# Kernel optimization log

Hardware: AMD Instinct MI355X
Metric: run time of the kernel (lower is better)

Reference implementation:

```python
import jax, jax.numpy as jnp
import numpy as np
from jax import lax

T_STEPS = 16
TAU = 2.0
ALPHA = 4.0  # sigmoid surrogate sharpness
BN_EPS = 1e-5


def conv1d(x, w, b, stride, pad):
    # x: [N,C,L], w: [O,I,K]
    y = lax.conv_general_dilated(x, w, (stride,), [(pad, pad)],
                                 dimension_numbers=('NCH', 'OIH', 'NCH'))
    return y + b[None, :, None]


def maxpool1d(x):  # kernel 3, stride 2, pad 1 (pad value -inf via init)
    return lax.reduce_window(x, -jnp.inf, lax.max, (1, 1, 3), (1, 1, 2),
                             [(0, 0), (0, 0), (1, 1)])


def spike(x):  # heaviside forward (surrogate only matters for bwd)
    return (x >= 0).astype(x.dtype)


def lif(x_seq):
    # multi-step LIF: v += (x - v)/tau (v_reset=0), spike at v>=1, hard reset, detach_reset
    def step(v, x):
        v = v + (x - v) / TAU
        s = spike(v - 1.0)
        v = v * (1.0 - lax.stop_gradient(s))
        return v, s
    _, s_seq = lax.scan(step, jnp.zeros_like(x_seq[0]), x_seq)
    return s_seq


def seq_apply(f, xs):
    # apply stateless layer over [T,B,...] by folding T into batch
    T, B = xs.shape[0], xs.shape[1]
    y = f(xs.reshape((T * B,) + xs.shape[2:]))
    return y.reshape((T, B) + y.shape[1:])


def setup_inputs() -> dict:
    key = jax.random.key(0)
    ks = jax.random.split(key, 12)
    B, L = 256, 4097
    inp = {
        'x': jax.random.normal(ks[0], (B, L), jnp.float32),
        'conv0_w': jax.random.normal(ks[1], (16, 1, 7), jnp.float32) * 0.2,
        'conv0_b': jax.random.normal(ks[2], (16,), jnp.float32) * 0.1,
        'bn_g': jnp.ones((16,), jnp.float32),
        'bn_b': jnp.zeros((16,), jnp.float32),
        'bn_m': jax.random.normal(ks[3], (16,), jnp.float32) * 0.1,
        'bn_v': jnp.ones((16,), jnp.float32),
        'conv1_w': jax.random.normal(ks[4], (32, 16, 5), jnp.float32) * 0.1,
        'conv1_b': jax.random.normal(ks[5], (32,), jnp.float32) * 0.1,
        'conv2_w': jax.random.normal(ks[6], (64, 32, 3), jnp.float32) * 0.1,
        'conv2_b': jax.random.normal(ks[7], (64,), jnp.float32) * 0.1,
        'fc1_w': jax.random.normal(ks[8], (32, 64), jnp.float32) * 0.12,
        'fc1_b': jax.random.normal(ks[9], (32,), jnp.float32) * 0.1,
        'fc2_w': jax.random.normal(ks[10], (5, 32), jnp.float32) * 0.17,
        'fc2_b': jax.random.normal(ks[11], (5,), jnp.float32) * 0.1,
    }
    return inp


def reference(x, conv0_w, conv0_b, bn_g, bn_b, bn_m, bn_v,
              conv1_w, conv1_b, conv2_w, conv2_b,
              fc1_w, fc1_b, fc2_w, fc2_b):
    # ---- static encoder ----
    h = x[:, None, :]                                  # [B,1,4097]
    h = conv1d(h, conv0_w, conv0_b, 2, 3)              # [B,16,2049]
    h = (h - bn_m[None, :, None]) * lax.rsqrt(bn_v + BN_EPS)[None, :, None] \
        * bn_g[None, :, None] + bn_b[None, :, None]
    h = jax.nn.relu(h)
    h = maxpool1d(h)                                   # [B,16,1025]
    # ---- repeat over T timesteps ----
    hs = jnp.broadcast_to(h[None], (T_STEPS,) + h.shape)  # [T,B,16,1025]
    # ---- spiking trunk ----
    hs = seq_apply(lambda a: conv1d(a, conv1_w, conv1_b, 2, 2), hs)  # [T,B,32,513]
    hs = lif(hs)
    hs = seq_apply(maxpool1d, hs)                      # [T,B,32,257]
    hs = seq_apply(lambda a: conv1d(a, conv2_w, conv2_b, 2, 1), hs)  # [T,B,64,129]
    hs = lif(hs)
    # dropout: identity (inference); adaptive avg pool to 1 + flatten
    hs = hs.mean(axis=-1)                              # [T,B,64]
    # ---- classifier ----
    hs = jnp.einsum('tbd,od->tbo', hs, fc1_w) + fc1_b  # [T,B,32]
    hs = lif(hs)
    hs = jnp.einsum('tbd,od->tbo', hs, fc2_w) + fc2_b  # [T,B,5]
    return hs.mean(axis=0)                             # [B,5]
```

## Files before the change

kernel.cpp:

```cpp
#include <hip/hip_runtime.h>
#include <math.h>


#define NB 256
#define LX 4097
#define LQ 2049
#define LP 1025
#define LJ1 513
#define LP1 257
#define LJ2 129

#define M1S 520
#define S2R 132

typedef float f32x4 __attribute__((ext_vector_type(4)));

__global__ __launch_bounds__(256) void kA_conv0(const float* __restrict__ x,
                                                const float* __restrict__ w0,
                                                const float* __restrict__ b0,
                                                const float* __restrict__ bng,
                                                const float* __restrict__ bnb,
                                                const float* __restrict__ bnm,
                                                const float* __restrict__ bnv,
                                                float* __restrict__ h,
                                                const float* __restrict__ w1,
                                                const float* __restrict__ w2,
                                                float* __restrict__ w1t,
                                                float* __restrict__ w2t) {
  __shared__ float xs[828];
  __shared__ float rs_l[16];
  int bid = blockIdx.x;
  int b = bid / 5, pt = bid % 5;
  int P0 = pt * 205;
  int tid = threadIdx.x;
  if (tid < 16) rs_l[tid] = (float)(1.0 / sqrt((double)bnv[tid] + 1e-5));
  const float* xb = x + (size_t)b * LX;
  int x0 = 4 * P0 - 5;
  for (int i = tid; i < 828; i += 256) {
    int gi = x0 + i;
    xs[i] = (gi >= 0 && gi < LX) ? xb[gi] : 0.f;
  }
  __syncthreads();
  if (tid < 205) {
    int p = P0 + tid;
    float win[12];
    {
      const f32x4* xv = (const f32x4*)xs;
      f32x4 a = xv[tid];
      f32x4 bq = xv[tid + 1];
      f32x4 cq = xv[tid + 2];
      win[0] = a.x; win[1] = a.y; win[2] = a.z; win[3] = a.w;
      win[4] = bq.x; win[5] = bq.y; win[6] = bq.z; win[7] = bq.w;
      win[8] = cq.x; win[9] = cq.y; win[10] = cq.z; win[11] = cq.w;
    }
    for (int c = 0; c < 16; ++c) {
      float wv[7];
#pragma unroll
      for (int k = 0; k < 7; ++k) wv[k] = w0[c * 7 + k];
      float rs = rs_l[c], g = bng[c], bb = bnb[c], m = bnm[c], bc = b0[c];
      float hm = -INFINITY;
#pragma unroll
      for (int dq = -1; dq <= 1; ++dq) {
        int q = 2 * p + dq;
        if (q < 0 || q >= LQ) continue;
        float s = 0.f;
        int base = 2 * dq + 2;
#pragma unroll
        for (int k = 0; k < 7; ++k) s = fmaf(win[base + k], wv[k], s);
        float y = s + bc;
        y = (y - m) * rs * g + bb;
        y = fmaxf(y, 0.f);
        hm = fmaxf(hm, y);
      }
      h[((size_t)b * 16 + c) * LP + p] = hm;
    }
  }
  if (bid < 16) {
    for (int idx = bid * 256 + tid; idx < 32 * 16 * 5; idx += 4096) {
      int k = idx % 5; int r = idx / 5; int ic = r % 16; int c = r / 16;
      w1t[(ic * 5 + k) * 32 + c] = w1[idx];
    }
    for (int idx = bid * 256 + tid; idx < 64 * 32 * 3; idx += 4096) {
      int k = idx % 3; int r = idx / 3; int c = r % 32; int oc = r / 32;
      w2t[(c * 3 + k) * 64 + oc] = w2[idx];
    }
  }
}

__global__ __launch_bounds__(256) void kB_conv1_lif(const float* __restrict__ h,
                                                    const float* __restrict__ w1t_g,
                                                    const float* __restrict__ b1,
                                                    unsigned short* __restrict__ m1) {
  __shared__ float hs[16 * 260];
  __shared__ float wl[16 * 5 * 32];
  int bid = blockIdx.x;
  int b = bid / 5, jt = bid % 5;
  int J0 = jt * 128;
  int tid = threadIdx.x;
  int c = tid & 31, jg = tid >> 5;

  {
    const float* hb = h + (size_t)b * 16 * LP;
    int p0 = 2 * J0 - 2;
    for (int i = tid; i < 16 * 260; i += 256) {
      int ic = i / 260, q = i - ic * 260;
      int p = p0 + q;
      hs[i] = (p >= 0 && p < LP) ? hb[ic * LP + p] : 0.f;
    }
    for (int i = tid; i < 2560; i += 256) wl[i] = w1t_g[i];
  }
  __syncthreads();
  int jbase = J0 + jg * 16;
  if (jbase > 512) return;

  float acc[16];
#pragma unroll
  for (int i = 0; i < 16; ++i) acc[i] = 0.f;

  for (int ic = 0; ic < 16; ++ic) {
    float win[36];
    const f32x4* row = (const f32x4*)(hs + ic * 260 + 32 * jg);
#pragma unroll
    for (int i = 0; i < 9; ++i) {
      f32x4 v = row[i];
      win[4 * i] = v.x; win[4 * i + 1] = v.y; win[4 * i + 2] = v.z; win[4 * i + 3] = v.w;
    }
    float wv[5];
#pragma unroll
    for (int k = 0; k < 5; ++k) wv[k] = wl[(ic * 5 + k) * 32 + c];
#pragma unroll
    for (int j = 0; j < 16; ++j) {
#pragma unroll
      for (int k = 0; k < 5; ++k) acc[j] = fmaf(win[2 * j + k], wv[k], acc[j]);
    }
  }

  float bc = b1[c];
  unsigned mskv[16];
#pragma unroll
  for (int j = 0; j < 16; ++j) {
    float xin = acc[j] + bc;
    float v = 0.f; unsigned mm = 0;
#pragma unroll
    for (int t = 0; t < 16; ++t) {
      v = v + (xin - v) * 0.5f;
      if (v >= 1.f) { mm |= (1u << t); v = 0.f; }
    }
    mskv[j] = mm;
  }
  size_t rowo = ((size_t)b * 32 + c) * M1S + jbase;
  if (jbase + 15 < LJ1) {
    uint4 u0, u1;
    u0.x = mskv[0] | (mskv[1] << 16);
    u0.y = mskv[2] | (mskv[3] << 16);
    u0.z = mskv[4] | (mskv[5] << 16);
    u0.w = mskv[6] | (mskv[7] << 16);
    u1.x = mskv[8] | (mskv[9] << 16);
    u1.y = mskv[10] | (mskv[11] << 16);
    u1.z = mskv[12] | (mskv[13] << 16);
    u1.w = mskv[14] | (mskv[15] << 16);
    *(uint4*)(m1 + rowo) = u0;
    *(uint4*)(m1 + rowo + 8) = u1;
  } else {
    for (int j = 0; j < 16; ++j)
      if (jbase + j < LJ1) m1[rowo + j] = (unsigned short)mskv[j];
  }
}

__global__ __launch_bounds__(256) void kD_conv2_lif(const unsigned short* __restrict__ m1,
                                                    const float* __restrict__ w2t_g,
                                                    const float* __restrict__ b2,
                                                    unsigned short* __restrict__ s2) {
  __shared__ __align__(16) float F[32 * 9 * 16];
  __shared__ unsigned mval[32 * 9];
  __shared__ unsigned short mbuf[32 * 20];
  int bid = blockIdx.x;
  int b = bid / 33, jt = bid % 33;
  int j0 = jt * 4;
  int tid = threadIdx.x;
  int w = tid >> 6;
  int lane = tid & 63;

  const unsigned short* m1b = m1 + (size_t)b * 32 * M1S;
  int qbase = 4 * j0 - 3;
  for (int i = tid; i < 1024; i += 256) {
    int c = i >> 5, u = i & 31;
    if (u < 20) {
      int q = qbase + u;
      mbuf[c * 20 + u] = (q >= 0 && q <= 512) ? m1b[(size_t)c * M1S + q] : (unsigned short)0;
    }
  }
  __syncthreads();

  for (int it = tid; it < 288; it += 256) {
    int c = it / 9, idx = it - c * 9;
    int p = 2 * j0 - 1 + idx;
    unsigned m = 0;
    if (p >= 0 && p < LP1) {
      const unsigned short* mr = mbuf + c * 20;
      int l0 = 2 * idx;
      m = (unsigned)mr[l0] | (unsigned)mr[l0 + 1] | (unsigned)mr[l0 + 2];
    }
    mval[it] = m;
    f32x4* Fr = (f32x4*)(F + it * 16);
    f32x4 f0, f1, f2, f3;
    f0.x = (float)(m & 1u);         f0.y = (float)((m >> 1) & 1u);
    f0.z = (float)((m >> 2) & 1u);  f0.w = (float)((m >> 3) & 1u);
    f1.x = (float)((m >> 4) & 1u);  f1.y = (float)((m >> 5) & 1u);
    f1.z = (float)((m >> 6) & 1u);  f1.w = (float)((m >> 7) & 1u);
    f2.x = (float)((m >> 8) & 1u);  f2.y = (float)((m >> 9) & 1u);
    f2.z = (float)((m >> 10) & 1u); f2.w = (float)((m >> 11) & 1u);
    f3.x = (float)((m >> 12) & 1u); f3.y = (float)((m >> 13) & 1u);
    f3.z = (float)((m >> 14) & 1u); f3.w = (float)((m >> 15) & 1u);
    Fr[0] = f0; Fr[1] = f1; Fr[2] = f2; Fr[3] = f3;
  }
  __syncthreads();

  float acc[16];
#pragma unroll
  for (int t = 0; t < 16; ++t) acc[t] = 0.f;

  const float* wrow = w2t_g + lane;
  for (int c = 0; c < 32; ++c) {
    int base9 = c * 9 + 2 * w;
    unsigned mv0 = mval[base9];
    unsigned mv1 = mval[base9 + 1];
    unsigned mv2 = mval[base9 + 2];
    if ((mv0 | mv1 | mv2) == 0u) continue;
    const float* wr = wrow + c * 192;
    const f32x4* Fb = (const f32x4*)(F + base9 * 16);
    if (mv0) {
      float wv = wr[0];
      f32x4 fv[4];
      fv[0] = Fb[0]; fv[1] = Fb[1]; fv[2] = Fb[2]; fv[3] = Fb[3];
#pragma unroll
      for (int t = 0; t < 16; ++t) acc[t] = fmaf(wv, fv[t >> 2][t & 3], acc[t]);
    }
    if (mv1) {
      float wv = wr[64];
      f32x4 fv[4];
      fv[0] = Fb[4]; fv[1] = Fb[5]; fv[2] = Fb[6]; fv[3] = Fb[7];
#pragma unroll
      for (int t = 0; t < 16; ++t) acc[t] = fmaf(wv, fv[t >> 2][t & 3], acc[t]);
    }
    if (mv2) {
      float wv = wr[128];
      f32x4 fv[4];
      fv[0] = Fb[8]; fv[1] = Fb[9]; fv[2] = Fb[10]; fv[3] = Fb[11];
#pragma unroll
      for (int t = 0; t < 16; ++t) acc[t] = fmaf(wv, fv[t >> 2][t & 3], acc[t]);
    }
  }

  int j = j0 + w;
  if (j < LJ2) {
    float bc = b2[lane];
    float v = 0.f; unsigned mm = 0;
#pragma unroll
    for (int t = 0; t < 16; ++t) {
      float xin = acc[t] + bc;
      v = v + (xin - v) * 0.5f;
      if (v >= 1.f) { mm |= (1u << t); v = 0.f; }
    }
    s2[((size_t)b * S2R + j) * 64 + lane] = (unsigned short)mm;
  }
}

__global__ __launch_bounds__(256) void kE_head(const unsigned short* __restrict__ s2,
                                               const float* __restrict__ fc1w,
                                               const float* __restrict__ fc1b,
                                               const float* __restrict__ fc2w,
                                               const float* __restrict__ fc2b,
                                               float* __restrict__ out) {
  __shared__ float meanL[16][64];
  __shared__ unsigned s3m[32];
  int b = blockIdx.x;
  int tid = threadIdx.x;
  int oc = tid >> 2, part = tid & 3;

  int jstart = (part == 0) ? 0 : 33 + (part - 1) * 32;
  int jcount = (part == 0) ? 33 : 32;
  const unsigned short* base = s2 + (size_t)b * S2R * 64 + oc;
  int cnt[16];
#pragma unroll
  for (int t = 0; t < 16; ++t) cnt[t] = 0;
  for (int u = 0; u < jcount; ++u) {
    unsigned m = base[(size_t)(jstart + u) * 64];
#pragma unroll
    for (int t = 0; t < 16; ++t) cnt[t] += (int)((m >> t) & 1u);
  }
#pragma unroll
  for (int t = 0; t < 16; ++t) {
    cnt[t] += __shfl_xor(cnt[t], 1);
    cnt[t] += __shfl_xor(cnt[t], 2);
  }
  if (part == 0) {
#pragma unroll
    for (int t = 0; t < 16; ++t) meanL[t][oc] = (float)cnt[t] / 129.f;
  }
  __syncthreads();

  if (tid < 32) {
    int o = tid;
    const float* wrow = fc1w + o * 64;
    float bb = fc1b[o];
    float v = 0.f;
    unsigned msk = 0;
    for (int t = 0; t < 16; ++t) {
      float s = 0.f;
      for (int d = 0; d < 64; ++d) s = fmaf(meanL[t][d], wrow[d], s);
      float xin = s + bb;
      v = v + (xin - v) * 0.5f;
      if (v >= 1.f) { msk |= (1u << t); v = 0.f; }
    }
    s3m[o] = msk;
  }
  __syncthreads();

  if (tid < 5) {
    int q = tid;
    const float* wrow = fc2w + q * 32;
    float bb = fc2b[q];
    float accs = 0.f;
    for (int t = 0; t < 16; ++t) {
      float s = 0.f;
      for (int o = 0; o < 32; ++o) s += (((s3m[o] >> t) & 1u) ? wrow[o] : 0.f);
      accs += (s + bb);
    }
    out[b * 5 + q] = accs / 16.f;
  }
}

extern "C" void kernel_launch(void* const* d_in, const int* in_sizes, int n_in,
                              void* d_out, int out_size, void* d_ws, size_t ws_size,
                              hipStream_t stream) {
  const float* x   = (const float*)d_in[0];
  const float* w0  = (const float*)d_in[1];
  const float* b0  = (const float*)d_in[2];
  const float* bng = (const float*)d_in[3];
  const float* bnb = (const float*)d_in[4];
  const float* bnm = (const float*)d_in[5];
  const float* bnv = (const float*)d_in[6];
  const float* w1  = (const float*)d_in[7];
  const float* b1  = (const float*)d_in[8];
  const float* w2  = (const float*)d_in[9];
  const float* b2  = (const float*)d_in[10];
  const float* f1w = (const float*)d_in[11];
  const float* f1b = (const float*)d_in[12];
  const float* f2w = (const float*)d_in[13];
  const float* f2b = (const float*)d_in[14];
  float* out = (float*)d_out;

  char* ws = (char*)d_ws;
  size_t sz_h  = (size_t)NB * 16 * LP * 4;
  size_t sz_m1 = (size_t)NB * 32 * M1S * 2;
  size_t sz_s2 = (size_t)NB * S2R * 64 * 2;
  size_t off_m1 = sz_h;
  size_t off_s2 = off_m1 + sz_m1;
  size_t off_sm = off_s2 + sz_s2;
  size_t sz_sm = (2560 + 6144) * 4;
  if (ws_size < off_sm + sz_sm) return;

  float* h = (float*)ws;
  unsigned short* m1 = (unsigned short*)(ws + off_m1);
  unsigned short* s2 = (unsigned short*)(ws + off_s2);
  float* w1t = (float*)(ws + off_sm);
  float* w2t = w1t + 2560;

  kA_conv0<<<NB * 5, 256, 0, stream>>>(x, w0, b0, bng, bnb, bnm, bnv, h, w1, w2, w1t, w2t);
  kB_conv1_lif<<<NB * 5, 256, 0, stream>>>(h, w1t, b1, m1);
  kD_conv2_lif<<<NB * 33, 256, 0, stream>>>(m1, w2t, b2, s2);
  kE_head<<<NB, 256, 0, stream>>>(s2, f1w, f1b, f2w, f2b, out);
}
```

Before: 131.6 us.

## Fuse conv0 encoder into conv1+LIF kernel and ballot-skip empty channels in conv2

The conv0+BN+ReLU+maxpool stage is now computed per tile directly into shared memory inside the conv1+LIF kernel. This removes the global h intermediate (about 16.8 MB write and read) and one kernel launch, and conv1 weights are transposed in shared memory instead of by a separate pass. The price is recomputing halo columns of conv0 for each tile. In conv2, a wave ballot builds a mask of non-empty input channels so the loop visits only active channels, and the F rows are padded to stride 20, likely to reduce LDS bank conflicts.

```diff
diff --git a/kernel.cpp b/kernel.cpp
--- a/kernel.cpp
+++ b/kernel.cpp
@@ -12,53 +12,72 @@
 
 #define M1S 520
 #define S2R 132
+#define HSW 260
 
 typedef float f32x4 __attribute__((ext_vector_type(4)));
 
-__global__ __launch_bounds__(256) void kA_conv0(const float* __restrict__ x,
+__global__ __launch_bounds__(256) void kF_front(const float* __restrict__ x,
                                                 const float* __restrict__ w0,
                                                 const float* __restrict__ b0,
                                                 const float* __restrict__ bng,
                                                 const float* __restrict__ bnb,
                                                 const float* __restrict__ bnm,
                                                 const float* __restrict__ bnv,
-                                                float* __restrict__ h,
                                                 const float* __restrict__ w1,
+                                                const float* __restrict__ b1,
+                                                unsigned short* __restrict__ m1,
                                                 const float* __restrict__ w2,
-                                                float* __restrict__ w1t,
                                                 float* __restrict__ w2t) {
-  __shared__ float xs[828];
+  __shared__ __align__(16) float xs[1052];
+  __shared__ __align__(16) float hs[16 * HSW];
+  __shared__ __align__(16) float wl[2560];
+  __shared__ float w0s[112];
+  __shared__ float cpar[64];
   __shared__ float rs_l[16];
   int bid = blockIdx.x;
-  int b = bid / 5, pt = bid % 5;
-  int P0 = pt * 205;
+  int b = bid / 5, jt = bid % 5;
+  int J0 = jt * 128;
+  int Pstart = 2 * J0 - 2;
   int tid = threadIdx.x;
+
   if (tid < 16) rs_l[tid] = (float)(1.0 / sqrt((double)bnv[tid] + 1e-5));
-  const float* xb = x + (size_t)b * LX;
-  int x0 = 4 * P0 - 5;
-  for (int i = tid; i < 828; i += 256) {
-    int gi = x0 + i;
-    xs[i] = (gi >= 0 && gi < LX) ? xb[gi] : 0.f;
-  }
-  __syncthreads();
-  if (tid < 205) {
-    int p = P0 + tid;
-    float win[12];
-    {
-      const f32x4* xv = (const f32x4*)xs;
-      f32x4 a = xv[tid];
-      f32x4 bq = xv[tid + 1];
-      f32x4 cq = xv[tid + 2];
-      win[0] = a.x; win[1] = a.y; win[2] = a.z; win[3] = a.w;
-      win[4] = bq.x; win[5] = bq.y; win[6] = bq.z; win[7] = bq.w;
-      win[8] = cq.x; win[9] = cq.y; win[10] = cq.z; win[11] = cq.w;
-    }
-    for (int c = 0; c < 16; ++c) {
+  {
+    const float* xb = x + (size_t)b * LX;
+    int xoff = 4 * Pstart - 5;
+    for (int i = tid; i < 1052; i += 256) {
+      int gi = xoff + i;
+      xs[i] = (gi >= 0 && gi < LX) ? xb[gi] : 0.f;
+    }
+    for (int i = tid; i < 2560; i += 256) {
+      int c = i & 31, r = i >> 5;
+      wl[i] = w1[c * 80 + r];
+    }
+    if (tid < 112) w0s[tid] = w0[tid];
+    if (tid >= 128 && tid < 192) {
+      int i = tid - 128;
+      int c = i >> 2, e = i & 3;
+      float v = (e == 0) ? bnm[c] : (e == 1) ? bng[c] : (e == 2) ? bnb[c] : b0[c];
+      cpar[i] = v;
+    }
+  }
+  __syncthreads();
+
+  for (int item = tid; item < 16 * 261; item += 256) {
+    int c = item / 261, dp = item - c * 261;
+    int p = Pstart + dp;
+    float hm = 0.f;
+    if (p >= 0 && p < LP) {
+      const f32x4* xv = (const f32x4*)(xs + 4 * dp);
+      f32x4 a = xv[0], bq = xv[1], cq = xv[2];
+      float win[12] = {a.x, a.y, a.z, a.w, bq.x, bq.y, bq.z, bq.w,
+                       cq.x, cq.y, cq.z, cq.w};
+      float m = cpar[4 * c], g = cpar[4 * c + 1], bb = cpar[4 * c + 2],
+            bc = cpar[4 * c + 3];
+      float rs = rs_l[c];
       float wv[7];
 #pragma unroll
-      for (int k = 0; k < 7; ++k) wv[k] = w0[c * 7 + k];
-      float rs = rs_l[c], g = bng[c], bb = bnb[c], m = bnm[c], bc = b0[c];
-      float hm = -INFINITY;
+      for (int k = 0; k < 7; ++k) wv[k] = w0s[c * 7 + k];
+      float best = -INFINITY;
 #pragma unroll
       for (int dq = -1; dq <= 1; ++dq) {
         int q = 2 * p + dq;
@@ -70,100 +89,79 @@
         float y = s + bc;
         y = (y - m) * rs * g + bb;
         y = fmaxf(y, 0.f);
-        hm = fmaxf(hm, y);
+        best = fmaxf(best, y);
       }
-      h[((size_t)b * 16 + c) * LP + p] = hm;
-    }
-  }
+      hm = best;
+    }
+    hs[c * HSW + dp] = hm;
+  }
+  __syncthreads();
+
+  {
+    int c = tid & 31, jg = tid >> 5;
+    int jbase = J0 + jg * 16;
+    if (jbase <= 512) {
+      float acc[16];
+#pragma unroll
+      for (int i = 0; i < 16; ++i) acc[i] = 0.f;
+
+      for (int ic = 0; ic < 16; ++ic) {
+        float win[36];
+        const f32x4* row = (const f32x4*)(hs + ic * HSW + 32 * jg);
+#pragma unroll
+        for (int i = 0; i < 9; ++i) {
+          f32x4 v = row[i];
+          win[4 * i] = v.x; win[4 * i + 1] = v.y;
+          win[4 * i + 2] = v.z; win[4 * i + 3] = v.w;
+        }
+        float wv[5];
+#pragma unroll
+        for (int k = 0; k < 5; ++k) wv[k] = wl[(ic * 5 + k) * 32 + c];
+#pragma unroll
+        for (int j = 0; j < 16; ++j) {
+#pragma unroll
+          for (int k = 0; k < 5; ++k) acc[j] = fmaf(win[2 * j + k], wv[k], acc[j]);
+        }
+      }
+
+      float bc = b1[c];
+      unsigned mskv[16];
+#pragma unroll
+      for (int j = 0; j < 16; ++j) {
+        float xin = acc[j] + bc;
+        float v = 0.f; unsigned mm = 0;
+#pragma unroll
+        for (int t = 0; t < 16; ++t) {
+          v = v + (xin - v) * 0.5f;
+          if (v >= 1.f) { mm |= (1u << t); v = 0.f; }
+        }
+        mskv[j] = mm;
+      }
+      size_t rowo = ((size_t)b * 32 + c) * M1S + jbase;
+      if (jbase + 15 < LJ1) {
+        uint4 u0, u1;
+        u0.x = mskv[0] | (mskv[1] << 16);
+        u0.y = mskv[2] | (mskv[3] << 16);
+        u0.z = mskv[4] | (mskv[5] << 16);
+        u0.w = mskv[6] | (mskv[7] << 16);
+        u1.x = mskv[8] | (mskv[9] << 16);
+        u1.y = mskv[10] | (mskv[11] << 16);
+        u1.z = mskv[12] | (mskv[13] << 16);
+        u1.w = mskv[14] | (mskv[15] << 16);
+        *(uint4*)(m1 + rowo) = u0;
+        *(uint4*)(m1 + rowo + 8) = u1;
+      } else {
+        for (int j = 0; j < 16; ++j)
+          if (jbase + j < LJ1) m1[rowo + j] = (unsigned short)mskv[j];
+      }
+    }
+  }
+
   if (bid < 16) {
-    for (int idx = bid * 256 + tid; idx < 32 * 16 * 5; idx += 4096) {
-      int k = idx % 5; int r = idx / 5; int ic = r % 16; int c = r / 16;
-      w1t[(ic * 5 + k) * 32 + c] = w1[idx];
-    }
     for (int idx = bid * 256 + tid; idx < 64 * 32 * 3; idx += 4096) {
       int k = idx % 3; int r = idx / 3; int c = r % 32; int oc = r / 32;
       w2t[(c * 3 + k) * 64 + oc] = w2[idx];
     }
-  }
-}
-
-__global__ __launch_bounds__(256) void kB_conv1_lif(const float* __restrict__ h,
-                                                    const float* __restrict__ w1t_g,
-                                                    const float* __restrict__ b1,
-                                                    unsigned short* __restrict__ m1) {
-  __shared__ float hs[16 * 260];
-  __shared__ float wl[16 * 5 * 32];
-  int bid = blockIdx.x;
-  int b = bid / 5, jt = bid % 5;
-  int J0 = jt * 128;
-  int tid = threadIdx.x;
-  int c = tid & 31, jg = tid >> 5;
-
-  {
-    const float* hb = h + (size_t)b * 16 * LP;
-    int p0 = 2 * J0 - 2;
-    for (int i = tid; i < 16 * 260; i += 256) {
-      int ic = i / 260, q = i - ic * 260;
-      int p = p0 + q;
-      hs[i] = (p >= 0 && p < LP) ? hb[ic * LP + p] : 0.f;
-    }
-    for (int i = tid; i < 2560; i += 256) wl[i] = w1t_g[i];
-  }
-  __syncthreads();
-  int jbase = J0 + jg * 16;
-  if (jbase > 512) return;
-
-  float acc[16];
-#pragma unroll
-  for (int i = 0; i < 16; ++i) acc[i] = 0.f;
-
-  for (int ic = 0; ic < 16; ++ic) {
-    float win[36];
-    const f32x4* row = (const f32x4*)(hs + ic * 260 + 32 * jg);
-#pragma unroll
-    for (int i = 0; i < 9; ++i) {
-      f32x4 v = row[i];
-      win[4 * i] = v.x; win[4 * i + 1] = v.y; win[4 * i + 2] = v.z; win[4 * i + 3] = v.w;
-    }
-    float wv[5];
-#pragma unroll
-    for (int k = 0; k < 5; ++k) wv[k] = wl[(ic * 5 + k) * 32 + c];
-#pragma unroll
-    for (int j = 0; j < 16; ++j) {
-#pragma unroll
-      for (int k = 0; k < 5; ++k) acc[j] = fmaf(win[2 * j + k], wv[k], acc[j]);
-    }
-  }
-
-  float bc = b1[c];
-  unsigned mskv[16];
-#pragma unroll
-  for (int j = 0; j < 16; ++j) {
-    float xin = acc[j] + bc;
-    float v = 0.f; unsigned mm = 0;
-#pragma unroll
-    for (int t = 0; t < 16; ++t) {
-      v = v + (xin - v) * 0.5f;
-      if (v >= 1.f) { mm |= (1u << t); v = 0.f; }
-    }
-    mskv[j] = mm;
-  }
-  size_t rowo = ((size_t)b * 32 + c) * M1S + jbase;
-  if (jbase + 15 < LJ1) {
-    uint4 u0, u1;
-    u0.x = mskv[0] | (mskv[1] << 16);
-    u0.y = mskv[2] | (mskv[3] << 16);
-    u0.z = mskv[4] | (mskv[5] << 16);
-    u0.w = mskv[6] | (mskv[7] << 16);
-    u1.x = mskv[8] | (mskv[9] << 16);
-    u1.y = mskv[10] | (mskv[11] << 16);
-    u1.z = mskv[12] | (mskv[13] << 16);
-    u1.w = mskv[14] | (mskv[15] << 16);
-    *(uint4*)(m1 + rowo) = u0;
-    *(uint4*)(m1 + rowo + 8) = u1;
-  } else {
-    for (int j = 0; j < 16; ++j)
-      if (jbase + j < LJ1) m1[rowo + j] = (unsigned short)mskv[j];
   }
 }
 
@@ -171,8 +169,8 @@
                                                     const float* __restrict__ w2t_g,
                                                     const float* __restrict__ b2,
                                                     unsigned short* __restrict__ s2) {
-  __shared__ __align__(16) float F[32 * 9 * 16];
-  __shared__ unsigned mval[32 * 9];
+  __shared__ __align__(16) float F[288 * 20];
+  __shared__ unsigned mval[288];
   __shared__ unsigned short mbuf[32 * 20];
   int bid = blockIdx.x;
   int b = bid / 33, jt = bid % 33;
@@ -202,7 +200,7 @@
       m = (unsigned)mr[l0] | (unsigned)mr[l0 + 1] | (unsigned)mr[l0 + 2];
     }
     mval[it] = m;
-    f32x4* Fr = (f32x4*)(F + it * 16);
+    f32x4* Fr = (f32x4*)(F + it * 20);
     f32x4 f0, f1, f2, f3;
     f0.x = (float)(m & 1u);         f0.y = (float)((m >> 1) & 1u);
     f0.z = (float)((m >> 2) & 1u);  f0.w = (float)((m >> 3) & 1u);
@@ -216,37 +214,51 @@
   }
   __syncthreads();
 
+  unsigned bits;
+  {
+    bool nz = false;
+    if (lane < 32) {
+      int base9 = lane * 9 + 2 * w;
+      nz = (mval[base9] | mval[base9 + 1] | mval[base9 + 2]) != 0u;
+    }
+    bits = (unsigned)__ballot(nz);
+  }
+
   float acc[16];
 #pragma unroll
   for (int t = 0; t < 16; ++t) acc[t] = 0.f;
 
   const float* wrow = w2t_g + lane;
-  for (int c = 0; c < 32; ++c) {
+  while (bits) {
+    int c = __builtin_ctz(bits);
+    bits &= bits - 1;
     int base9 = c * 9 + 2 * w;
     unsigned mv0 = mval[base9];
     unsigned mv1 = mval[base9 + 1];
     unsigned mv2 = mval[base9 + 2];
-    if ((mv0 | mv1 | mv2) == 0u) continue;
     const float* wr = wrow + c * 192;
-    const f32x4* Fb = (const f32x4*)(F + base9 * 16);
+    const float* Fb = F + base9 * 20;
     if (mv0) {
       float wv = wr[0];
+      const f32x4* Fp = (const f32x4*)Fb;
       f32x4 fv[4];
-      fv[0] = Fb[0]; fv[1] = Fb[1]; fv[2] = Fb[2]; fv[3] = Fb[3];
+      fv[0] = Fp[0]; fv[1] = Fp[1]; fv[2] = Fp[2]; fv[3] = Fp[3];
 #pragma unroll
       for (int t = 0; t < 16; ++t) acc[t] = fmaf(wv, fv[t >> 2][t & 3], acc[t]);
     }
     if (mv1) {
       float wv = wr[64];
+      const f32x4* Fp = (const f32x4*)(Fb + 20);
       f32x4 fv[4];
-      fv[0] = Fb[4]; fv[1] = Fb[5]; fv[2] = Fb[6]; fv[3] = Fb[7];
+      fv[0] = Fp[0]; fv[1] = Fp[1]; fv[2] = Fp[2]; fv[3] = Fp[3];
 #pragma unroll
       for (int t = 0; t < 16; ++t) acc[t] = fmaf(wv, fv[t >> 2][t & 3], acc[t]);
     }
     if (mv2) {
       float wv = wr[128];
+      const f32x4* Fp = (const f32x4*)(Fb + 40);
       f32x4 fv[4];
-      fv[0] = Fb[8]; fv[1] = Fb[9]; fv[2] = Fb[10]; fv[3] = Fb[11];
+      fv[0] = Fp[0]; fv[1] = Fp[1]; fv[2] = Fp[2]; fv[3] = Fp[3];
 #pragma unroll
       for (int t = 0; t < 16; ++t) acc[t] = fmaf(wv, fv[t >> 2][t & 3], acc[t]);
     }
@@ -352,23 +364,17 @@
   float* out = (float*)d_out;
 
   char* ws = (char*)d_ws;
-  size_t sz_h  = (size_t)NB * 16 * LP * 4;
   size_t sz_m1 = (size_t)NB * 32 * M1S * 2;
   size_t sz_s2 = (size_t)NB * S2R * 64 * 2;
-  size_t off_m1 = sz_h;
-  size_t off_s2 = off_m1 + sz_m1;
-  size_t off_sm = off_s2 + sz_s2;
-  size_t sz_sm = (2560 + 6144) * 4;
-  if (ws_size < off_sm + sz_sm) return;
-
-  float* h = (float*)ws;
-  unsigned short* m1 = (unsigned short*)(ws + off_m1);
+  size_t off_s2 = sz_m1;
+  size_t off_w2 = off_s2 + sz_s2;
+  if (ws_size < off_w2 + 6144 * 4) return;
+
+  unsigned short* m1 = (unsigned short*)ws;
   unsigned short* s2 = (unsigned short*)(ws + off_s2);
-  float* w1t = (float*)(ws + off_sm);
-  float* w2t = w1t + 2560;
-
-  kA_conv0<<<NB * 5, 256, 0, stream>>>(x, w0, b0, bng, bnb, bnm, bnv, h, w1, w2, w1t, w2t);
-  kB_conv1_lif<<<NB * 5, 256, 0, stream>>>(h, w1t, b1, m1);
+  float* w2t = (float*)(ws + off_w2);
+
+  kF_front<<<NB * 5, 256, 0, stream>>>(x, w0, b0, bng, bnb, bnm, bnv, w1, b1, m1, w2, w2t);
   kD_conv2_lif<<<NB * 33, 256, 0, stream>>>(m1, w2t, b2, s2);
   kE_head<<<NB, 256, 0, stream>>>(s2, f1w, f1b, f2w, f2b, out);
 }
```

Measured after the change: 121.1 us. 8.0% less time.
